# Kernel tuning notes

Measured on AMD Instinct MI355X. Metric: run time of the kernel, lower is better.

The kernel has to match this reference:

```python
import jax, jax.numpy as jnp
import numpy as np


def setup_inputs() -> dict:
    key = jax.random.key(0)
    k1, k2, k3, k4 = jax.random.split(key, 4)
    B, S, I, O, G = 4, 2048, 4096, 11008, 128
    x = jax.random.normal(k1, (B, S, I), dtype=jnp.float32)
    # unpacked int4 codes in [0, 16)
    weight_q = jax.random.randint(k2, (O, I), 0, 16, dtype=jnp.int32)
    scales = jax.random.uniform(k3, (I // G, O, 1), minval=0.001, maxval=0.02)
    zeros = jax.random.normal(k4, (I // G, O, 1)) * 0.01
    scales_and_zeros = jnp.concatenate([scales, zeros], axis=-1).astype(jnp.bfloat16)
    return {"x": x, "weight_q": weight_q, "scales_and_zeros": scales_and_zeros, "groupsize": G}


def reference(x, weight_q, scales_and_zeros, groupsize):
    # Dequantize: w[o, g*gs + j] = (q - 8) * scale[g, o] + zero[g, o], in bf16
    O, I = weight_q.shape
    G = I // groupsize
    q = weight_q.reshape(O, G, groupsize).astype(jnp.bfloat16)  # [O, G, gs]
    s = scales_and_zeros[:, :, 0].T[:, :, None]  # [O, G, 1]
    z = scales_and_zeros[:, :, 1].T[:, :, None]  # [O, G, 1]
    w = ((q - 8.0) * s + z).reshape(O, I)  # bf16 dequantized weight
    xb = x.astype(jnp.bfloat16).reshape(-1, I)
    y = jnp.matmul(xb, w.T)  # [N, O] in bf16 (matches precision=bf16)
    y = y.astype(x.dtype)
    return y.reshape(x.shape[:-1] + (O,))
```

## Files before the change

### kernel.cpp

```cpp
#include <hip/hip_runtime.h>
#include <cstdint>
#include <cstddef>

#define N_ 8192
#define K_ 4096
#define O_ 11008
#define NT_ (K_ / 32)

typedef __bf16 bf16x8 __attribute__((ext_vector_type(8)));
typedef float f32x4 __attribute__((ext_vector_type(4)));

__device__ __forceinline__ uint16_t f2bf(float f) {
    uint32_t u = __float_as_uint(f);
    u += 0x7fffu + ((u >> 16) & 1u);
    return (uint16_t)(u >> 16);
}
__device__ __forceinline__ float bf2f(uint16_t b) {
    return __uint_as_float(((uint32_t)b) << 16);
}
__device__ __forceinline__ float bfr(float f) { return bf2f(f2bf(f)); }

__device__ __forceinline__ void async_cp16(const uint16_t* gsrc, uint16_t* ldst) {
    __builtin_amdgcn_global_load_lds(
        (__attribute__((address_space(1))) void*)gsrc,
        (__attribute__((address_space(3))) void*)ldst, 16, 0, 0);
}

__global__ __launch_bounds__(256) void xcast(const float* __restrict__ X,
                                             uint16_t* __restrict__ Xb) {
    const size_t n4 = (size_t)N_ * K_ / 4;
    size_t i = (size_t)blockIdx.x * 256u + threadIdx.x;
    const size_t stride = (size_t)gridDim.x * 256u;
    for (; i < n4; i += stride) {
        float4 a = ((const float4*)X)[i];
        union { uint16_t u[4]; uint2 v; } r;
        r.u[0] = f2bf(a.x); r.u[1] = f2bf(a.y);
        r.u[2] = f2bf(a.z); r.u[3] = f2bf(a.w);
        ((uint2*)Xb)[i] = r.v;
    }
}

__global__ __launch_bounds__(256) void wdeq(const int* __restrict__ Q,
                                            const float* __restrict__ SZ,
                                            uint16_t* __restrict__ Wb) {
    const size_t n4 = (size_t)O_ * K_ / 4;
    size_t i = (size_t)blockIdx.x * 256u + threadIdx.x;
    const size_t stride = (size_t)gridDim.x * 256u;
    for (; i < n4; i += stride) {
        const size_t e = i * 4;
        const size_t o = e >> 12;
        const uint32_t g = ((uint32_t)e >> 7) & 31;
        const float2 sz = ((const float2*)SZ)[(size_t)g * O_ + o];
        const float s = bfr(sz.x);
        const float z = bfr(sz.y);
        int4 q = ((const int4*)Q)[i];
        union { uint16_t u[4]; uint2 v; } r;
        r.u[0] = f2bf(bfr((float)(q.x - 8) * s) + z);
        r.u[1] = f2bf(bfr((float)(q.y - 8) * s) + z);
        r.u[2] = f2bf(bfr((float)(q.z - 8) * s) + z);
        r.u[3] = f2bf(bfr((float)(q.w - 8) * s) + z);
        ((uint2*)Wb)[i] = r.v;
    }
}

__global__ __launch_bounds__(512, 2) void gemm_mfma8p(const uint16_t* __restrict__ A,
                                                      const uint16_t* __restrict__ B,
                                                      float* __restrict__ C) {
    __shared__ uint16_t sA[4][256 * 32];
    __shared__ uint16_t sB[4][256 * 32];

    const int tid = threadIdx.x;
    const int l = tid & 63;
    const int w = tid >> 6;
    const int wm = w >> 2;
    const int wn = w & 3;
    const int n0 = blockIdx.x * 256;
    const int o0 = blockIdx.y * 256;

    const int gk = (((tid & 3) ^ ((tid >> 3) & 3)) & 3) * 8;
    const int sr0 = tid >> 2;
    const uint16_t* gA0 = A + (size_t)(n0 + sr0) * K_ + gk;
    const uint16_t* gA1 = A + (size_t)(n0 + 128 + sr0) * K_ + gk;
    const uint16_t* gB0 = B + (size_t)(o0 + sr0) * K_ + gk;
    const uint16_t* gB1 = B + (size_t)(o0 + 128 + sr0) * K_ + gk;
    const int ldst = tid * 8;

    const int lr = l & 15;
    const int cph = (((l >> 4) ^ ((l >> 1) & 3)) & 3) * 8;

    f32x4 acc[8][4] = {};

#define STAGE_A(j)                                                      \
    {                                                                   \
        const size_t ko = (size_t)(j) * 32;                             \
        uint16_t* d = &sA[(j) & 3][ldst];                               \
        async_cp16(gA0 + ko, d);                                        \
        async_cp16(gA1 + ko, d + 4096);                                 \
    }
#define STAGE_B(j)                                                      \
    {                                                                   \
        const size_t ko = (size_t)(j) * 32;                             \
        uint16_t* d = &sB[(j) & 3][ldst];                               \
        async_cp16(gB0 + ko, d);                                        \
        async_cp16(gB1 + ko, d + 4096);                                 \
    }

    STAGE_A(0) STAGE_B(0)
    STAGE_A(1) STAGE_B(1)
    STAGE_A(2) STAGE_B(2)

    for (int j = 0; j < NT_; ++j) {
        if (j < NT_ - 2)       asm volatile("s_waitcnt vmcnt(8)" ::: "memory");
        else if (j == NT_ - 2) asm volatile("s_waitcnt vmcnt(4)" ::: "memory");
        else                   asm volatile("s_waitcnt vmcnt(0)" ::: "memory");
        __builtin_amdgcn_s_barrier();
        __builtin_amdgcn_sched_barrier(0);

        const uint16_t* tA = sA[j & 3];
        const uint16_t* tB = sB[j & 3];

        bf16x8 bfrag[4], afrag[4];
#pragma unroll
        for (int n = 0; n < 4; ++n)
            bfrag[n] = *(const bf16x8*)&tB[(wn * 64 + n * 16 + lr) * 32 + cph];
#pragma unroll
        for (int m = 0; m < 4; ++m)
            afrag[m] = *(const bf16x8*)&tA[(wm * 128 + m * 16 + lr) * 32 + cph];
        if (j < NT_ - 3) STAGE_A(j + 3)
        __builtin_amdgcn_s_barrier();
        __builtin_amdgcn_sched_barrier(0);
        __builtin_amdgcn_s_setprio(1);
#pragma unroll
        for (int m = 0; m < 4; ++m)
#pragma unroll
            for (int n = 0; n < 4; ++n)
                acc[m][n] = __builtin_amdgcn_mfma_f32_16x16x32_bf16(afrag[m], bfrag[n], acc[m][n], 0, 0, 0);
        __builtin_amdgcn_s_setprio(0);
        __builtin_amdgcn_s_barrier();
        __builtin_amdgcn_sched_barrier(0);

#pragma unroll
        for (int m = 0; m < 4; ++m)
            afrag[m] = *(const bf16x8*)&tA[(wm * 128 + 64 + m * 16 + lr) * 32 + cph];
        if (j < NT_ - 3) STAGE_B(j + 3)
        __builtin_amdgcn_s_barrier();
        __builtin_amdgcn_sched_barrier(0);
        __builtin_amdgcn_s_setprio(1);
#pragma unroll
        for (int m = 0; m < 4; ++m)
#pragma unroll
            for (int n = 0; n < 4; ++n)
                acc[m + 4][n] = __builtin_amdgcn_mfma_f32_16x16x32_bf16(afrag[m], bfrag[n], acc[m + 4][n], 0, 0, 0);
        __builtin_amdgcn_s_setprio(0);
    }
#undef STAGE_A
#undef STAGE_B

    const int rbase = (l >> 4) * 4;
#pragma unroll
    for (int m = 0; m < 8; ++m) {
#pragma unroll
        for (int n = 0; n < 4; ++n) {
#pragma unroll
            for (int r = 0; r < 4; ++r) {
                const size_t row = (size_t)(n0 + wm * 128 + m * 16 + rbase + r);
                C[row * O_ + (o0 + wn * 64 + n * 16 + lr)] = bfr(acc[m][n][r]);
            }
        }
    }
}

__global__ __launch_bounds__(256) void gemm_probe_f32sz(const float* __restrict__ X,
                                                        const int* __restrict__ Q,
                                                        const float* __restrict__ SZf,
                                                        float* __restrict__ C) {
    __shared__ float xs[32][64];
    __shared__ float ws[32][64];
    const int tid = threadIdx.x;
    const int n0 = blockIdx.x * 64;
    const int o0 = blockIdx.y * 64;
    const int tn = tid >> 4;
    const int to = tid & 15;
    const int srow = tid >> 2;
    const int skq = (tid & 3) * 8;

    float acc[4][4] = {};

    for (int k0 = 0; k0 < K_; k0 += 32) {
        {
            const float4* xp = (const float4*)(X + (size_t)(n0 + srow) * K_ + k0 + skq);
            float4 a = xp[0], b = xp[1];
            float v[8] = {a.x, a.y, a.z, a.w, b.x, b.y, b.z, b.w};
#pragma unroll
            for (int j = 0; j < 8; ++j) xs[skq + j][srow] = bfr(v[j]);
        }
        {
            const int o = o0 + srow;
            const uint32_t g = (uint32_t)k0 >> 7;
            const size_t p = (size_t)g * O_ + o;
            const float s = bfr(SZf[2 * p]);
            const float z = bfr(SZf[2 * p + 1]);
            const int4* qp = (const int4*)(Q + (size_t)o * K_ + k0 + skq);
            int4 qa = qp[0], qb = qp[1];
            int qs[8] = {qa.x, qa.y, qa.z, qa.w, qb.x, qb.y, qb.z, qb.w};
#pragma unroll
            for (int j = 0; j < 8; ++j) {
                float w1 = bfr((float)(qs[j] - 8) * s);
                ws[skq + j][srow] = bfr(w1 + z);
            }
        }
        __syncthreads();

#pragma unroll 8
        for (int kk = 0; kk < 32; ++kk) {
            const float4 xv = *(const float4*)&xs[kk][tn * 4];
            const float4 wv = *(const float4*)&ws[kk][to * 4];
            const float xa[4] = {xv.x, xv.y, xv.z, xv.w};
            const float wa[4] = {wv.x, wv.y, wv.z, wv.w};
#pragma unroll
            for (int i = 0; i < 4; ++i)
#pragma unroll
                for (int j = 0; j < 4; ++j)
                    acc[i][j] = fmaf(xa[i], wa[j], acc[i][j]);
        }
        __syncthreads();
    }

#pragma unroll
    for (int i = 0; i < 4; ++i) {
        const size_t row = (size_t)(n0 + tn * 4 + i);
#pragma unroll
        for (int j = 0; j < 4; ++j) {
            C[row * O_ + (o0 + to * 4 + j)] = bfr(acc[i][j]);
        }
    }
}

__global__ __launch_bounds__(256) void sentinel_fill(float* __restrict__ C, size_t n, float v) {
    size_t i = (size_t)blockIdx.x * 256u + threadIdx.x;
    size_t stride = (size_t)gridDim.x * 256u;
    for (; i < n; i += stride) C[i] = v;
}

extern "C" void kernel_launch(void* const* d_in, const int* in_sizes, int n_in,
                              void* d_out, int out_size, void* d_ws, size_t ws_size,
                              hipStream_t stream) {
    const float* x = (const float*)d_in[0];
    const int* q = (const int*)d_in[1];
    const float* szf = (const float*)d_in[2];
    float* out = (float*)d_out;

    float sentinel = 0.0f;
    if (n_in < 3)                         sentinel = 1000.0f;
    else if (in_sizes[0] != 33554432)     sentinel = 2000.0f;
    else if (in_sizes[1] != 45088768)     sentinel = 3000.0f;
    else if (in_sizes[2] != 704512)       sentinel = 4000.0f;
    else if (out_size   != 90177536)      sentinel = 5000.0f;

    if (sentinel != 0.0f) {
        sentinel_fill<<<8192, 256, 0, stream>>>(out, (size_t)out_size, sentinel);
        return;
    }

    const size_t xb_bytes = (size_t)N_ * K_ * 2;
    const size_t wb_bytes = (size_t)O_ * K_ * 2;

    if (ws_size >= xb_bytes + wb_bytes) {
        uint16_t* Xb = (uint16_t*)d_ws;
        uint16_t* Wb = (uint16_t*)((char*)d_ws + xb_bytes);
        xcast<<<2048, 256, 0, stream>>>(x, Xb);
        wdeq<<<2048, 256, 0, stream>>>(q, szf, Wb);
        dim3 grid(N_ / 256, O_ / 256);
        gemm_mfma8p<<<grid, 512, 0, stream>>>(Xb, Wb, out);
    } else {
        dim3 grid(N_ / 64, O_ / 64);
        gemm_probe_f32sz<<<grid, 256, 0, stream>>>(x, q, szf, out);
    }
}
```

Baseline: 1.314 ms.

## Collapse GEMM inner loop to one barrier phase and widen cast kernels

The GEMM main loop now runs each K-tile in a single phase instead of two half-phases. It loads all eight A fragments at once, issues both A and B async copies together, and drops the extra barriers and sched_barriers. This cuts synchronisation and barrier stalls per tile, at the cost of more live VGPRs for fragments and less explicit control over how loads and MFMAs interleave. The input cast and weight dequant kernels now process eight elements per thread with 16-byte stores and a doubled grid, to reduce per-element overhead.

```diff
diff --git a/kernel.cpp b/kernel.cpp
--- a/kernel.cpp
+++ b/kernel.cpp
@@ -28,42 +28,45 @@
 
 __global__ __launch_bounds__(256) void xcast(const float* __restrict__ X,
                                              uint16_t* __restrict__ Xb) {
-    const size_t n4 = (size_t)N_ * K_ / 4;
+    const size_t n8 = (size_t)N_ * K_ / 8;
     size_t i = (size_t)blockIdx.x * 256u + threadIdx.x;
     const size_t stride = (size_t)gridDim.x * 256u;
-    for (; i < n4; i += stride) {
-        float4 a = ((const float4*)X)[i];
-        union { uint16_t u[4]; uint2 v; } r;
-        r.u[0] = f2bf(a.x); r.u[1] = f2bf(a.y);
-        r.u[2] = f2bf(a.z); r.u[3] = f2bf(a.w);
-        ((uint2*)Xb)[i] = r.v;
+    for (; i < n8; i += stride) {
+        float4 a = ((const float4*)X)[2 * i];
+        float4 b = ((const float4*)X)[2 * i + 1];
+        union { uint16_t u[8]; uint4 v; } r;
+        r.u[0] = f2bf(a.x); r.u[1] = f2bf(a.y); r.u[2] = f2bf(a.z); r.u[3] = f2bf(a.w);
+        r.u[4] = f2bf(b.x); r.u[5] = f2bf(b.y); r.u[6] = f2bf(b.z); r.u[7] = f2bf(b.w);
+        ((uint4*)Xb)[i] = r.v;
     }
 }
 
 __global__ __launch_bounds__(256) void wdeq(const int* __restrict__ Q,
                                             const float* __restrict__ SZ,
                                             uint16_t* __restrict__ Wb) {
-    const size_t n4 = (size_t)O_ * K_ / 4;
+    const size_t n8 = (size_t)O_ * K_ / 8;
     size_t i = (size_t)blockIdx.x * 256u + threadIdx.x;
     const size_t stride = (size_t)gridDim.x * 256u;
-    for (; i < n4; i += stride) {
-        const size_t e = i * 4;
+    for (; i < n8; i += stride) {
+        const size_t e = i * 8;
         const size_t o = e >> 12;
         const uint32_t g = ((uint32_t)e >> 7) & 31;
         const float2 sz = ((const float2*)SZ)[(size_t)g * O_ + o];
         const float s = bfr(sz.x);
         const float z = bfr(sz.y);
-        int4 q = ((const int4*)Q)[i];
-        union { uint16_t u[4]; uint2 v; } r;
-        r.u[0] = f2bf(bfr((float)(q.x - 8) * s) + z);
-        r.u[1] = f2bf(bfr((float)(q.y - 8) * s) + z);
-        r.u[2] = f2bf(bfr((float)(q.z - 8) * s) + z);
-        r.u[3] = f2bf(bfr((float)(q.w - 8) * s) + z);
-        ((uint2*)Wb)[i] = r.v;
-    }
-}
-
-__global__ __launch_bounds__(512, 2) void gemm_mfma8p(const uint16_t* __restrict__ A,
+        int4 qa = ((const int4*)Q)[2 * i];
+        int4 qb = ((const int4*)Q)[2 * i + 1];
+        int qs[8] = {qa.x, qa.y, qa.z, qa.w, qb.x, qb.y, qb.z, qb.w};
+        union { uint16_t u[8]; uint4 v; } r;
+#pragma unroll
+        for (int j = 0; j < 8; ++j) {
+            r.u[j] = f2bf(bfr((float)(qs[j] - 8) * s) + z);
+        }
+        ((uint4*)Wb)[i] = r.v;
+    }
+}
+
+__global__ __launch_bounds__(512, 2) void gemm_mfma1b(const uint16_t* __restrict__ A,
                                                       const uint16_t* __restrict__ B,
                                                       float* __restrict__ C) {
     __shared__ uint16_t sA[4][256 * 32];
@@ -114,43 +117,27 @@
         else if (j == NT_ - 2) asm volatile("s_waitcnt vmcnt(4)" ::: "memory");
         else                   asm volatile("s_waitcnt vmcnt(0)" ::: "memory");
         __builtin_amdgcn_s_barrier();
-        __builtin_amdgcn_sched_barrier(0);
 
         const uint16_t* tA = sA[j & 3];
         const uint16_t* tB = sB[j & 3];
 
-        bf16x8 bfrag[4], afrag[4];
+        bf16x8 bfrag[4], afrag[8];
 #pragma unroll
         for (int n = 0; n < 4; ++n)
             bfrag[n] = *(const bf16x8*)&tB[(wn * 64 + n * 16 + lr) * 32 + cph];
 #pragma unroll
-        for (int m = 0; m < 4; ++m)
+        for (int m = 0; m < 8; ++m)
             afrag[m] = *(const bf16x8*)&tA[(wm * 128 + m * 16 + lr) * 32 + cph];
-        if (j < NT_ - 3) STAGE_A(j + 3)
-        __builtin_amdgcn_s_barrier();
-        __builtin_amdgcn_sched_barrier(0);
+        if (j < NT_ - 3) {
+            STAGE_A(j + 3)
+            STAGE_B(j + 3)
+        }
         __builtin_amdgcn_s_setprio(1);
 #pragma unroll
-        for (int m = 0; m < 4; ++m)
+        for (int m = 0; m < 8; ++m)
 #pragma unroll
             for (int n = 0; n < 4; ++n)
                 acc[m][n] = __builtin_amdgcn_mfma_f32_16x16x32_bf16(afrag[m], bfrag[n], acc[m][n], 0, 0, 0);
-        __builtin_amdgcn_s_setprio(0);
-        __builtin_amdgcn_s_barrier();
-        __builtin_amdgcn_sched_barrier(0);
-
-#pragma unroll
-        for (int m = 0; m < 4; ++m)
-            afrag[m] = *(const bf16x8*)&tA[(wm * 128 + 64 + m * 16 + lr) * 32 + cph];
-        if (j < NT_ - 3) STAGE_B(j + 3)
-        __builtin_amdgcn_s_barrier();
-        __builtin_amdgcn_sched_barrier(0);
-        __builtin_amdgcn_s_setprio(1);
-#pragma unroll
-        for (int m = 0; m < 4; ++m)
-#pragma unroll
-            for (int n = 0; n < 4; ++n)
-                acc[m + 4][n] = __builtin_amdgcn_mfma_f32_16x16x32_bf16(afrag[m], bfrag[n], acc[m + 4][n], 0, 0, 0);
         __builtin_amdgcn_s_setprio(0);
     }
 #undef STAGE_A
@@ -268,10 +255,10 @@
     if (ws_size >= xb_bytes + wb_bytes) {
         uint16_t* Xb = (uint16_t*)d_ws;
         uint16_t* Wb = (uint16_t*)((char*)d_ws + xb_bytes);
-        xcast<<<2048, 256, 0, stream>>>(x, Xb);
-        wdeq<<<2048, 256, 0, stream>>>(q, szf, Wb);
+        xcast<<<4096, 256, 0, stream>>>(x, Xb);
+        wdeq<<<4096, 256, 0, stream>>>(q, szf, Wb);
         dim3 grid(N_ / 256, O_ / 256);
-        gemm_mfma8p<<<grid, 512, 0, stream>>>(Xb, Wb, out);
+        gemm_mfma1b<<<grid, 512, 0, stream>>>(Xb, Wb, out);
     } else {
         dim3 grid(N_ / 64, O_ / 64);
         gemm_probe_f32sz<<<grid, 256, 0, stream>>>(x, q, szf, out);
```

Measured after the change: 1.244 ms. -5.3%, faster.
